# Kernel tuning notes

Measured on AMD Instinct MI355X. Metric: run time of the kernel, lower is better.

The kernel has to match this reference:

```python
import jax, jax.numpy as jnp
import numpy as np

B, S, I, H = 64, 1024, 512, 512

def setup_inputs() -> dict:
    key = jax.random.key(0)
    ks = jax.random.split(key, 9)
    sd = 1.0 / np.sqrt(H)  # match torch uniform(-sd, sd) scale roughly
    return {
        "x": jax.random.normal(ks[0], (B, S, I), dtype=jnp.float32),
        "h0": jnp.zeros((B, H), dtype=jnp.float32),
        "c0": jnp.zeros((B, H), dtype=jnp.float32),
        "W_xh": jax.random.normal(ks[1], (I + H, 4 * H), dtype=jnp.float32) * sd,
        "W_ci": jax.random.normal(ks[2], (H,), dtype=jnp.float32) * sd,
        "W_cf": jax.random.normal(ks[3], (H,), dtype=jnp.float32) * sd,
        "W_co": jax.random.normal(ks[4], (H,), dtype=jnp.float32) * sd,
        "b_i": jax.random.normal(ks[5], (H,), dtype=jnp.float32) * sd,
        "b_f": jax.random.normal(ks[6], (H,), dtype=jnp.float32) * sd,
        "b_c": jax.random.normal(ks[7], (H,), dtype=jnp.float32) * sd,
        "b_o": jax.random.normal(ks[8], (H,), dtype=jnp.float32) * sd,
    }

def reference(x, h0, c0, W_xh, W_ci, W_cf, W_co, b_i, b_f, b_c, b_o):
    # cat([x_t, h_t]) @ W_xh == x_t @ W_x + h_t @ W_h; precompute the input GEMM.
    in_dim = x.shape[-1]
    W_x, W_h = W_xh[:in_dim], W_xh[in_dim:]
    zx = jnp.einsum('bsi,ig->bsg', x, W_x)  # [B, S, 4H]

    def step(carry, zx_t):
        h, c = carry
        z = zx_t + h @ W_h  # [B, 4H]
        z_i, z_f, z_c, z_o = jnp.split(z, 4, axis=-1)
        i_t = jax.nn.sigmoid(z_i + c * W_ci + b_i)
        f_t = jax.nn.sigmoid(z_f + c * W_cf + b_f)
        c_new = f_t * c + i_t * jnp.tanh(z_c + b_c)
        o_t = jax.nn.sigmoid(z_o + c_new * W_co + b_o)
        h_new = o_t * jnp.tanh(c_new)
        return (h_new, c_new), h_new

    (h_T, c_T), hs = jax.lax.scan(step, (h0, c0), jnp.swapaxes(zx, 0, 1))
    hidden_seq = jnp.swapaxes(hs, 0, 1)  # [B, S, H]
    return hidden_seq, h_T, c_T
```

## Files before the change

kernel.cpp:

```cpp
#include <hip/hip_runtime.h>
#include <hip/hip_fp16.h>
#include <stdint.h>
#include <stddef.h>

#define Bb 64
#define Ss 1024
#define Ii 512
#define Hh 512
#define G4 2048
#define NBK 64
#define JPB 8

typedef _Float16 h16;
typedef _Float16 h16x8 __attribute__((ext_vector_type(8)));
typedef float    f32x4 __attribute__((ext_vector_type(4)));
typedef unsigned u32x4 __attribute__((ext_vector_type(4)));

__device__ __forceinline__ float sigm(float x){ return 1.0f / (1.0f + __expf(-x)); }
__device__ __forceinline__ float tanh_(float x){
  float e = __expf(-2.0f * fabsf(x));
  float t = (1.0f - e) / (1.0f + e);
  return copysignf(t, x);
}

__device__ __forceinline__ u32x4 load_coh16(const void* p){
  u32x4 r;
  asm volatile("global_load_dwordx4 %0, %1, off sc0 sc1"
               : "=v"(r) : "v"(p) : "memory");
  return r;
}
__device__ __forceinline__ void store_coh2(void* p, unsigned v){
  asm volatile("global_store_short %0, %1, off sc0 sc1"
               :: "v"(p), "v"(v) : "memory");
}
__device__ __forceinline__ u32x4 load_once16(const void* p){
  u32x4 r;
  asm volatile("global_load_dwordx4 %0, %1, off"
               : "=v"(r) : "v"(p) : "memory");
  return r;
}

__device__ __forceinline__ int hfrag_off(int b, int j){
  return ((b >> 4) * 16 + (j >> 5)) * 512 + (((b & 15) | (((j >> 3) & 3) << 4)) << 3) + (j & 7);
}

__global__ void prep_weights(const float* __restrict__ Wxh, h16* __restrict__ WxT){
  int idx = blockIdx.x * 256 + threadIdx.x;
  if (idx >= Ii * G4) return;
  int k = idx / G4, n = idx % G4;
  WxT[(size_t)n * Ii + k] = (h16)Wxh[idx];
}

__global__ void prep_rec(const float* __restrict__ Wxh, u32x4* __restrict__ Wr,
                         const float* __restrict__ h0g,
                         unsigned short* __restrict__ hbuf){
  int blk = blockIdx.x, tid = threadIdx.x;
  if (blk < 512){
    int d  = blk * 256 + tid;
    int l  = d & 63, pk = (d >> 6) & 31, bk = d >> 11;
    int n  = pk >> 4, ks = pk & 15;
    int k  = ks * 32 + (l >> 4) * 8;
    int cl = n * 16 + (l & 15);
    int col = (cl >> 3) * 512 + bk * JPB + (cl & 7);
    h16x8 v;
    #pragma unroll
    for (int e = 0; e < 8; ++e)
      v[e] = (h16)Wxh[(size_t)(Ii + k + e) * G4 + col];
    Wr[d] = *(u32x4*)&v;
  } else {
    int t = (blk - 512) * 256 + tid;
    #pragma unroll
    for (int i = 0; i < 32; ++i){
      int idx = t * 32 + i;
      int b = idx >> 9, j = idx & 511;
      h16 v = (h16)h0g[idx];
      unsigned short bits = *(unsigned short*)&v;
      int off = hfrag_off(b, j);
      hbuf[off]           = (unsigned short)(bits & 0xFFFEu);
      hbuf[Bb * Hh + off] = (unsigned short)0x0001u;
    }
  }
}

#define BM 128
#define BN 128
#define BK 32
#define LDP 48

__global__ __launch_bounds__(256) void gemm_zx(const float* __restrict__ x,
                                               const h16* __restrict__ WxT,
                                               float* __restrict__ zx,
                                               int t0, int tclog){
  __shared__ h16 lA[BM][LDP];
  __shared__ h16 lB[BN][LDP];
  const int tid  = threadIdx.x;
  const int lane = tid & 63, wid = tid >> 6;
  const int wm = wid >> 1, wn = wid & 1;
  const int bn0 = blockIdx.x * BN, bm0 = blockIdx.y * BM;

  f32x4 acc[4][4] = {};

  const int r_local = tid >> 1;
  const int kh = (tid & 1) * 16;
  const int r = bm0 + r_local;
  const int bidx = r >> tclog;
  const int sc   = r & ((1 << tclog) - 1);
  const float* xrow = x + ((size_t)bidx * Ss + (t0 + sc)) * Ii + kh;

  for (int ks = 0; ks < Ii / BK; ++ks){
    const int k0 = ks * BK;
    __syncthreads();
    {
      const float* p = xrow + k0;
      f32x4 v0 = *(const f32x4*)(p);
      f32x4 v1 = *(const f32x4*)(p + 4);
      f32x4 v2 = *(const f32x4*)(p + 8);
      f32x4 v3 = *(const f32x4*)(p + 12);
      h16x8 o0, o1;
      o0[0]=(h16)v0[0]; o0[1]=(h16)v0[1]; o0[2]=(h16)v0[2]; o0[3]=(h16)v0[3];
      o0[4]=(h16)v1[0]; o0[5]=(h16)v1[1]; o0[6]=(h16)v1[2]; o0[7]=(h16)v1[3];
      o1[0]=(h16)v2[0]; o1[1]=(h16)v2[1]; o1[2]=(h16)v2[2]; o1[3]=(h16)v2[3];
      o1[4]=(h16)v3[0]; o1[5]=(h16)v3[1]; o1[6]=(h16)v3[2]; o1[7]=(h16)v3[3];
      *(h16x8*)&lA[r_local][kh]     = o0;
      *(h16x8*)&lA[r_local][kh + 8] = o1;
    }
    #pragma unroll
    for (int i = 0; i < 2; ++i){
      int flat = i * 256 + tid;
      int nl = flat >> 2, kq = flat & 3;
      u32x4 w = *(const u32x4*)(WxT + ((size_t)(bn0 + nl)) * Ii + k0 + kq * 8);
      *(u32x4*)&lB[nl][kq * 8] = w;
    }
    __syncthreads();
    h16x8 af[4], bfr[4];
    #pragma unroll
    for (int m = 0; m < 4; ++m)
      af[m] = *(const h16x8*)&lA[wm * 64 + m * 16 + (lane & 15)][(lane >> 4) * 8];
    #pragma unroll
    for (int n = 0; n < 4; ++n)
      bfr[n] = *(const h16x8*)&lB[wn * 64 + n * 16 + (lane & 15)][(lane >> 4) * 8];
    #pragma unroll
    for (int m = 0; m < 4; ++m)
      #pragma unroll
      for (int n = 0; n < 4; ++n)
        acc[m][n] = __builtin_amdgcn_mfma_f32_16x16x32_f16(af[m], bfr[n], acc[m][n], 0, 0, 0);
  }
  #pragma unroll
  for (int m = 0; m < 4; ++m){
    int rg = bm0 + wm * 64 + m * 16 + ((lane >> 4) << 2);
    #pragma unroll
    for (int n = 0; n < 4; ++n){
      int cg = bn0 + wn * 64 + n * 16 + (lane & 15);
      #pragma unroll
      for (int q = 0; q < 4; ++q)
        zx[(size_t)(rg + q) * G4 + cg] = acc[m][n][q];
    }
  }
}

__global__ __launch_bounds__(256, 1) void lstm_rec2(
    const float* __restrict__ zx, const u32x4* __restrict__ Wr,
    unsigned short* __restrict__ hbuf,
    const float* __restrict__ c0g, float* __restrict__ c_state,
    const float* __restrict__ Wci, const float* __restrict__ Wcf, const float* __restrict__ Wco,
    const float* __restrict__ bi, const float* __restrict__ bfg, const float* __restrict__ bc,
    const float* __restrict__ bo,
    float* __restrict__ out, float* __restrict__ hT, float* __restrict__ cT,
    int t0, int Tc, int first, int last)
{
  __shared__ float zf[64 * 33];
  __shared__ float szp[64 * 36];

  const int bk = blockIdx.x, tid = threadIdx.x;
  const int l = tid & 63, w = tid >> 6;
  const int jl = tid & 7, b0 = tid >> 3;
  const int jg = bk * JPB + jl;

  const float wci = Wci[jg], wcf = Wcf[jg], wco = Wco[jg];
  const float vbi = bi[jg], vbf = bfg[jg], vbc = bc[jg], vbo = bo[jg];

  float cA, cB;
  if (first){ cA = c0g[b0 * Hh + jg]; cB = c0g[(b0 + 32) * Hh + jg]; }
  else      { cA = c_state[b0 * Hh + jg]; cB = c_state[(b0 + 32) * Hh + jg]; }

  h16x8 bfr[32];
  {
    const u32x4* p = Wr + (size_t)bk * 2048 + l;
    #pragma unroll
    for (int pk = 0; pk < 32; ++pk){
      u32x4 t = load_once16(p + (size_t)pk * 64);
      bfr[pk] = *(h16x8*)&t;
    }
    asm volatile("s_waitcnt vmcnt(0)" ::: "memory");
  }

  const int bz = tid >> 2, gz = tid & 3;
  const float* zxbase = zx + (size_t)bz * Tc * G4 + gz * 512 + bk * JPB;
  float4 zc0 = *(const float4*)(zxbase);
  float4 zc1 = *(const float4*)(zxbase + 4);

  const int crow = w * 16 + (l >> 4) * 4;

  const int st_pk = bk >> 2;
  const int st_lhi = (bk & 3) << 4;
  const int ld_off = (w * 16) * 512 + l * 8;

  for (int s = 0; s < Tc; ++s){
    const int gs = t0 + s;
    const int par = gs & 1;

    float4 zn0, zn1;
    if (s + 1 < Tc){
      const float* p = zxbase + (size_t)(s + 1) * G4;
      zn0 = *(const float4*)p; zn1 = *(const float4*)(p + 4);
    }

    *(float4*)&szp[bz * 36 + gz * 8]     = zc0;
    *(float4*)&szp[bz * 36 + gz * 8 + 4] = zc1;

    const unsigned exp32 = (((unsigned)gs >> 1) & 1u) * 0x00010001u;
    const unsigned short* hp = hbuf + (size_t)par * (Bb * Hh) + ld_off;
    f32x4 acc0, acc1;
    for (;;){
      u32x4 hr[16];
      #pragma unroll
      for (int pk = 0; pk < 16; ++pk)
        hr[pk] = load_coh16(hp + pk * 512);
      asm volatile("s_waitcnt vmcnt(0)" ::: "memory");
      __builtin_amdgcn_sched_barrier(0);
      unsigned bad = 0;
      acc0 = (f32x4){0.f,0.f,0.f,0.f};
      acc1 = (f32x4){0.f,0.f,0.f,0.f};
      #pragma unroll
      for (int pk = 0; pk < 16; ++pk){
        u32x4 v = hr[pk];
        bad |= (v[0] ^ exp32) & 0x00010001u;
        bad |= (v[1] ^ exp32) & 0x00010001u;
        bad |= (v[2] ^ exp32) & 0x00010001u;
        bad |= (v[3] ^ exp32) & 0x00010001u;
        h16x8 a = *(h16x8*)&v;
        acc0 = __builtin_amdgcn_mfma_f32_16x16x32_f16(a, bfr[pk],      acc0, 0, 0, 0);
        acc1 = __builtin_amdgcn_mfma_f32_16x16x32_f16(a, bfr[16 + pk], acc1, 0, 0, 0);
      }
      if (__all(bad == 0)) break;
    }

    #pragma unroll
    for (int q = 0; q < 4; ++q){
      zf[(crow + q) * 33 + (l & 15)]      = acc0[q];
      zf[(crow + q) * 33 + 16 + (l & 15)] = acc1[q];
    }
    __syncthreads();

    const unsigned tagn = (((unsigned)(gs + 1) >> 1) & 1u);
    unsigned short* hdst = hbuf + (size_t)(par ^ 1) * (Bb * Hh);
    #pragma unroll
    for (int pr = 0; pr < 2; ++pr){
      const int b = b0 + pr * 32;
      float cp = pr ? cB : cA;
      float z_i = szp[b * 36 + jl]      + zf[b * 33 + jl];
      float z_f = szp[b * 36 + 8 + jl]  + zf[b * 33 + 8 + jl];
      float z_c = szp[b * 36 + 16 + jl] + zf[b * 33 + 16 + jl];
      float z_o = szp[b * 36 + 24 + jl] + zf[b * 33 + 24 + jl];
      float iv = sigm(z_i + cp * wci + vbi);
      float fv = sigm(z_f + cp * wcf + vbf);
      float cn = fv * cp + iv * tanh_(z_c + vbc);
      float ov = sigm(z_o + cn * wco + vbo);
      float hn = ov * tanh_(cn);
      if (pr) cB = cn; else cA = cn;
      h16 hh = (h16)hn;
      unsigned hbits = ((unsigned)*(unsigned short*)&hh & 0xFFFEu) | tagn;
      int off = ((b >> 4) * 16 + st_pk) * 512 + (((b & 15) | st_lhi) << 3) + jl;
      store_coh2(hdst + off, hbits);
      out[((size_t)b * Ss + gs) * Hh + jg] = hn;
      if (last && s == Tc - 1){ hT[b * Hh + jg] = hn; cT[b * Hh + jg] = cn; }
    }
    __syncthreads();

    zc0 = zn0; zc1 = zn1;
  }

  c_state[b0 * Hh + jg] = cA;
  c_state[(b0 + 32) * Hh + jg] = cB;
}

extern "C" void kernel_launch(void* const* d_in, const int* in_sizes, int n_in,
                              void* d_out, int out_size, void* d_ws, size_t ws_size,
                              hipStream_t stream){
  const float* x   = (const float*)d_in[0];
  const float* h0  = (const float*)d_in[1];
  const float* c0  = (const float*)d_in[2];
  const float* Wxh = (const float*)d_in[3];
  const float* Wci = (const float*)d_in[4];
  const float* Wcf = (const float*)d_in[5];
  const float* Wco = (const float*)d_in[6];
  const float* bi  = (const float*)d_in[7];
  const float* bf  = (const float*)d_in[8];
  const float* bc  = (const float*)d_in[9];
  const float* bo  = (const float*)d_in[10];

  float* out = (float*)d_out;
  float* hT  = out + (size_t)Bb * Ss * Hh;
  float* cT  = hT + (size_t)Bb * Hh;

  uint8_t* ws = (uint8_t*)d_ws;
  size_t off = 0;
  auto take = [&](size_t bytes) -> uint8_t* {
    uint8_t* p = ws + off;
    off += (bytes + 255) & ~(size_t)255;
    return p;
  };
  h16*            WxT     = (h16*)take((size_t)G4 * Ii * 2);
  u32x4*          Wr      = (u32x4*)take((size_t)G4 * Hh * 2);
  unsigned short* hbuf    = (unsigned short*)take((size_t)2 * Bb * Hh * 2);
  float*          c_state = (float*)take((size_t)Bb * Hh * 4);

  int Tc = Ss, tclog = 10;
  while (Tc > 2 && off + (size_t)Bb * Tc * G4 * 4 > ws_size){ Tc >>= 1; tclog--; }
  float* zxbuf = (float*)take((size_t)Bb * Tc * G4 * 4);

  prep_weights<<<(Ii * G4) / 256, 256, 0, stream>>>(Wxh, WxT);
  prep_rec<<<516, 256, 0, stream>>>(Wxh, Wr, h0, hbuf);

  int nch = Ss / Tc;
  for (int c = 0; c < nch; ++c){
    int t0 = c * Tc;
    dim3 grid(G4 / BN, Bb * Tc / BM);
    gemm_zx<<<grid, 256, 0, stream>>>(x, WxT, zxbuf, t0, tclog);
    lstm_rec2<<<NBK, 256, 0, stream>>>(zxbuf, Wr, hbuf, c0, c_state,
                                       Wci, Wcf, Wco, bi, bf, bc, bo,
                                       out, hT, cT, t0, Tc, c == 0, c == nch - 1);
  }
}
```

Measured before the change: 3.627 ms.

## Halve recurrent blocks, compute all four gates per lane without LDS or barriers

The recurrent kernel now uses 32 blocks of 16 hidden units each instead of 64 blocks of 8. Each wave issues four MFMAs per k-step so that one lane holds the i/f/c/o gate values for its own (batch, unit) pairs. This removes the shared-memory gate exchange and both __syncthreads per timestep, and the precomputed input projection is read straight into registers. In exchange, each block holds twice the recurrent weights in registers (64 fragments), half as many CUs take part in the sequential loop, and the weight preload now waits after every load.

```diff
diff --git a/kernel.cpp b/kernel.cpp
--- a/kernel.cpp
+++ b/kernel.cpp
@@ -8,8 +8,8 @@
 #define Ii 512
 #define Hh 512
 #define G4 2048
-#define NBK 64
-#define JPB 8
+#define NBK 32
+#define JPB 16
 
 typedef _Float16 h16;
 typedef _Float16 h16x8 __attribute__((ext_vector_type(8)));
@@ -33,9 +33,10 @@
   asm volatile("global_store_short %0, %1, off sc0 sc1"
                :: "v"(p), "v"(v) : "memory");
 }
-__device__ __forceinline__ u32x4 load_once16(const void* p){
+__device__ __forceinline__ u32x4 load_once16_drain(const void* p){
   u32x4 r;
-  asm volatile("global_load_dwordx4 %0, %1, off"
+  asm volatile("global_load_dwordx4 %0, %1, off\n\t"
+               "s_waitcnt vmcnt(0)"
                : "=v"(r) : "v"(p) : "memory");
   return r;
 }
@@ -57,11 +58,10 @@
   int blk = blockIdx.x, tid = threadIdx.x;
   if (blk < 512){
     int d  = blk * 256 + tid;
-    int l  = d & 63, pk = (d >> 6) & 31, bk = d >> 11;
+    int l  = d & 63, pk = (d >> 6) & 63, bk = d >> 12;
     int n  = pk >> 4, ks = pk & 15;
     int k  = ks * 32 + (l >> 4) * 8;
-    int cl = n * 16 + (l & 15);
-    int col = (cl >> 3) * 512 + bk * JPB + (cl & 7);
+    int col = n * 512 + bk * JPB + (l & 15);
     h16x8 v;
     #pragma unroll
     for (int e = 0; e < 8; ++e)
@@ -168,59 +168,62 @@
     float* __restrict__ out, float* __restrict__ hT, float* __restrict__ cT,
     int t0, int Tc, int first, int last)
 {
-  __shared__ float zf[64 * 33];
-  __shared__ float szp[64 * 36];
-
   const int bk = blockIdx.x, tid = threadIdx.x;
   const int l = tid & 63, w = tid >> 6;
-  const int jl = tid & 7, b0 = tid >> 3;
-  const int jg = bk * JPB + jl;
+  const int j15 = l & 15;
+  const int p4  = l >> 4;
+  const int jg  = bk * JPB + j15;
+  const int bbase = w * 16 + p4 * 4;
 
   const float wci = Wci[jg], wcf = Wcf[jg], wco = Wco[jg];
   const float vbi = bi[jg], vbf = bfg[jg], vbc = bc[jg], vbo = bo[jg];
 
-  float cA, cB;
-  if (first){ cA = c0g[b0 * Hh + jg]; cB = c0g[(b0 + 32) * Hh + jg]; }
-  else      { cA = c_state[b0 * Hh + jg]; cB = c_state[(b0 + 32) * Hh + jg]; }
-
-  h16x8 bfr[32];
+  float cst[4];
+  #pragma unroll
+  for (int q = 0; q < 4; ++q)
+    cst[q] = first ? c0g[(bbase + q) * Hh + jg] : c_state[(bbase + q) * Hh + jg];
+
+  h16x8 bfr[64];
   {
-    const u32x4* p = Wr + (size_t)bk * 2048 + l;
-    #pragma unroll
-    for (int pk = 0; pk < 32; ++pk){
-      u32x4 t = load_once16(p + (size_t)pk * 64);
+    const u32x4* p = Wr + (size_t)bk * 4096 + l;
+    #pragma unroll
+    for (int pk = 0; pk < 64; ++pk){
+      u32x4 t = load_once16_drain(p + (size_t)pk * 64);
       bfr[pk] = *(h16x8*)&t;
     }
-    asm volatile("s_waitcnt vmcnt(0)" ::: "memory");
-  }
-
-  const int bz = tid >> 2, gz = tid & 3;
-  const float* zxbase = zx + (size_t)bz * Tc * G4 + gz * 512 + bk * JPB;
-  float4 zc0 = *(const float4*)(zxbase);
-  float4 zc1 = *(const float4*)(zxbase + 4);
-
-  const int crow = w * 16 + (l >> 4) * 4;
-
-  const int st_pk = bk >> 2;
-  const int st_lhi = (bk & 3) << 4;
-  const int ld_off = (w * 16) * 512 + l * 8;
+  }
+
+  const float* zp[4];
+  #pragma unroll
+  for (int q = 0; q < 4; ++q)
+    zp[q] = zx + (size_t)(bbase + q) * Tc * G4 + jg;
+
+  float zc[16];
+  #pragma unroll
+  for (int q = 0; q < 4; ++q)
+    #pragma unroll
+    for (int n = 0; n < 4; ++n)
+      zc[q * 4 + n] = zp[q][n * 512];
+
+  const int ld_base = w * 8192 + l * 8;
+  const int soff0 = (w * 16 + (bk >> 1)) * 512
+                  + (((p4 << 2)) | ((((bk << 1) + (j15 >> 3)) & 3) << 4)) * 8 + (l & 7);
 
   for (int s = 0; s < Tc; ++s){
     const int gs = t0 + s;
     const int par = gs & 1;
 
-    float4 zn0, zn1;
-    if (s + 1 < Tc){
-      const float* p = zxbase + (size_t)(s + 1) * G4;
-      zn0 = *(const float4*)p; zn1 = *(const float4*)(p + 4);
-    }
-
-    *(float4*)&szp[bz * 36 + gz * 8]     = zc0;
-    *(float4*)&szp[bz * 36 + gz * 8 + 4] = zc1;
+    const int sn = (s + 1 < Tc) ? (s + 1) : s;
+    float zn[16];
+    #pragma unroll
+    for (int q = 0; q < 4; ++q)
+      #pragma unroll
+      for (int n = 0; n < 4; ++n)
+        zn[q * 4 + n] = zp[q][(size_t)sn * G4 + n * 512];
 
     const unsigned exp32 = (((unsigned)gs >> 1) & 1u) * 0x00010001u;
-    const unsigned short* hp = hbuf + (size_t)par * (Bb * Hh) + ld_off;
-    f32x4 acc0, acc1;
+    const unsigned short* hp = hbuf + (size_t)par * (Bb * Hh) + ld_base;
+    f32x4 a0, a1, a2, a3;
     for (;;){
       u32x4 hr[16];
       #pragma unroll
@@ -229,8 +232,10 @@
       asm volatile("s_waitcnt vmcnt(0)" ::: "memory");
       __builtin_amdgcn_sched_barrier(0);
       unsigned bad = 0;
-      acc0 = (f32x4){0.f,0.f,0.f,0.f};
-      acc1 = (f32x4){0.f,0.f,0.f,0.f};
+      a0 = (f32x4){0.f,0.f,0.f,0.f};
+      a1 = (f32x4){0.f,0.f,0.f,0.f};
+      a2 = (f32x4){0.f,0.f,0.f,0.f};
+      a3 = (f32x4){0.f,0.f,0.f,0.f};
       #pragma unroll
       for (int pk = 0; pk < 16; ++pk){
         u32x4 v = hr[pk];
@@ -239,49 +244,44 @@
         bad |= (v[2] ^ exp32) & 0x00010001u;
         bad |= (v[3] ^ exp32) & 0x00010001u;
         h16x8 a = *(h16x8*)&v;
-        acc0 = __builtin_amdgcn_mfma_f32_16x16x32_f16(a, bfr[pk],      acc0, 0, 0, 0);
-        acc1 = __builtin_amdgcn_mfma_f32_16x16x32_f16(a, bfr[16 + pk], acc1, 0, 0, 0);
+        a0 = __builtin_amdgcn_mfma_f32_16x16x32_f16(a, bfr[pk],      a0, 0, 0, 0);
+        a1 = __builtin_amdgcn_mfma_f32_16x16x32_f16(a, bfr[16 + pk], a1, 0, 0, 0);
+        a2 = __builtin_amdgcn_mfma_f32_16x16x32_f16(a, bfr[32 + pk], a2, 0, 0, 0);
+        a3 = __builtin_amdgcn_mfma_f32_16x16x32_f16(a, bfr[48 + pk], a3, 0, 0, 0);
       }
       if (__all(bad == 0)) break;
     }
 
+    const unsigned tagn = (((unsigned)(gs + 1) >> 1) & 1u);
+    unsigned short* hdst = hbuf + (size_t)(par ^ 1) * (Bb * Hh) + soff0;
     #pragma unroll
     for (int q = 0; q < 4; ++q){
-      zf[(crow + q) * 33 + (l & 15)]      = acc0[q];
-      zf[(crow + q) * 33 + 16 + (l & 15)] = acc1[q];
-    }
-    __syncthreads();
-
-    const unsigned tagn = (((unsigned)(gs + 1) >> 1) & 1u);
-    unsigned short* hdst = hbuf + (size_t)(par ^ 1) * (Bb * Hh);
-    #pragma unroll
-    for (int pr = 0; pr < 2; ++pr){
-      const int b = b0 + pr * 32;
-      float cp = pr ? cB : cA;
-      float z_i = szp[b * 36 + jl]      + zf[b * 33 + jl];
-      float z_f = szp[b * 36 + 8 + jl]  + zf[b * 33 + 8 + jl];
-      float z_c = szp[b * 36 + 16 + jl] + zf[b * 33 + 16 + jl];
-      float z_o = szp[b * 36 + 24 + jl] + zf[b * 33 + 24 + jl];
+      const int b = bbase + q;
+      float z_i = a0[q] + zc[q * 4 + 0];
+      float z_f = a1[q] + zc[q * 4 + 1];
+      float z_c = a2[q] + zc[q * 4 + 2];
+      float z_o = a3[q] + zc[q * 4 + 3];
+      float cp = cst[q];
       float iv = sigm(z_i + cp * wci + vbi);
       float fv = sigm(z_f + cp * wcf + vbf);
       float cn = fv * cp + iv * tanh_(z_c + vbc);
       float ov = sigm(z_o + cn * wco + vbo);
       float hn = ov * tanh_(cn);
-      if (pr) cB = cn; else cA = cn;
+      cst[q] = cn;
       h16 hh = (h16)hn;
       unsigned hbits = ((unsigned)*(unsigned short*)&hh & 0xFFFEu) | tagn;
-      int off = ((b >> 4) * 16 + st_pk) * 512 + (((b & 15) | st_lhi) << 3) + jl;
-      store_coh2(hdst + off, hbits);
+      store_coh2(hdst + q * 8, hbits);
       out[((size_t)b * Ss + gs) * Hh + jg] = hn;
       if (last && s == Tc - 1){ hT[b * Hh + jg] = hn; cT[b * Hh + jg] = cn; }
     }
-    __syncthreads();
-
-    zc0 = zn0; zc1 = zn1;
-  }
-
-  c_state[b0 * Hh + jg] = cA;
-  c_state[(b0 + 32) * Hh + jg] = cB;
+
+    #pragma unroll
+    for (int i = 0; i < 16; ++i) zc[i] = zn[i];
+  }
+
+  #pragma unroll
+  for (int q = 0; q < 4; ++q)
+    c_state[(bbase + q) * Hh + jg] = cst[q];
 }
 
 extern "C" void kernel_launch(void* const* d_in, const int* in_sizes, int n_in,
```

Result: slower. 4.956 ms (+36.6%).
